# Kernel tuning notes

Measured on AMD Instinct MI355X. Metric: run time of the kernel, lower is better.

The kernel has to match this reference:

```python
import jax, jax.numpy as jnp
import numpy as np

B, S, D_MODEL, D_INNER = 64, 128, 1024, 1024


def setup_inputs() -> dict:
    key = jax.random.key(0)
    ks = jax.random.split(key, 10)
    sc = 0.02
    return {
        "embeddings": jax.random.normal(ks[0], (B, S, D_MODEL), dtype=jnp.float32),
        "Wq": jax.random.normal(ks[1], (D_MODEL, D_INNER), dtype=jnp.float32) * sc,
        "bq": jnp.zeros((D_INNER,), dtype=jnp.float32),
        "Wk": jax.random.normal(ks[2], (D_MODEL, D_INNER), dtype=jnp.float32) * sc,
        "bk": jnp.zeros((D_INNER,), dtype=jnp.float32),
        "Wv": jax.random.normal(ks[3], (D_MODEL, D_INNER), dtype=jnp.float32) * sc,
        "bv": jnp.zeros((D_INNER,), dtype=jnp.float32),
        "w": jax.random.normal(ks[4], (S, S), dtype=jnp.float32) * sc,
        "Wo": jax.random.normal(ks[5], (D_INNER, D_MODEL), dtype=jnp.float32) * sc,
        "bo": jnp.zeros((D_MODEL,), dtype=jnp.float32),
    }


def reference(embeddings, Wq, bq, Wk, bk, Wv, bv, w, Wo, bo):
    # embeddings: [B, S, Dm]
    seq_len = embeddings.shape[1]
    q = embeddings @ Wq + bq          # [B, S, Di]
    k = embeddings @ Wk + bk
    v = embeddings @ Wv + bv

    max_k = jnp.max(k, axis=1, keepdims=True)   # [B, 1, Di]
    exp_k = jnp.exp(k - max_k)                  # [B, S, Di]

    max_w = jnp.max(w, axis=1, keepdims=True)   # [S, 1]
    wn = w - max_w                              # [S, S]
    tril = jnp.tril(jnp.ones((seq_len, seq_len), dtype=bool))
    wn = jnp.where(tril, wn[:seq_len, :seq_len], -jnp.inf)
    # torch.einsum('bjj,bjd->bjd', exp_w, x) picks the DIAGONAL of exp_w
    # (repeated subscript j) and multiplies elementwise along the seq dim.
    diag_w = jnp.exp(jnp.diagonal(wn))          # [S]; tril diagonal is True so finite
    dw = diag_w[None, :, None]                  # [1, S, 1]

    numerator = dw * (exp_k * v)                # [B, S, Di]
    denominator = dw * exp_k                    # [B, S, Di]
    out = jax.nn.sigmoid(q) * (numerator / denominator)
    return out @ Wo + bo                        # [B, S, Dm]
```

## Files before the change

### kernel.cpp

```cpp
#include <hip/hip_runtime.h>


typedef short bf16x8 __attribute__((ext_vector_type(8)));
typedef float f32x4  __attribute__((ext_vector_type(4)));

__device__ __forceinline__ short f2bf(float f) {
  union { float f; unsigned u; } x; x.f = f;
  unsigned r = x.u + 0x7fffu + ((x.u >> 16) & 1u);
  return (short)(r >> 16);
}

struct alignas(16) S8 { short v[8]; };

#define GLDS(g, l) \
  __builtin_amdgcn_global_load_lds((const __attribute__((address_space(1))) void*)(g), \
                                   (__attribute__((address_space(3))) void*)(l), 16, 0, 0)

__global__ __launch_bounds__(256) void prep_kernel(
    const float* __restrict__ emb, const float* __restrict__ Wq, const float* __restrict__ Wv,
    const float* __restrict__ Wo, short* __restrict__ embB, short* __restrict__ WqvT,
    short* __restrict__ WoT) {
  __shared__ float tr[32 * 33];
  const int t = threadIdx.x;
  const int bid = blockIdx.x;
  const int gdim = gridDim.x;

  for (size_t i = (size_t)bid * 256 + t; i < 1048576; i += (size_t)gdim * 256) {
    const float4* p = (const float4*)emb + i * 2;
    float4 a = p[0], b = p[1];
    S8 s;
    s.v[0] = f2bf(a.x); s.v[1] = f2bf(a.y); s.v[2] = f2bf(a.z); s.v[3] = f2bf(a.w);
    s.v[4] = f2bf(b.x); s.v[5] = f2bf(b.y); s.v[6] = f2bf(b.z); s.v[7] = f2bf(b.w);
    ((S8*)embB)[i] = s;
  }

  int tx = t & 31, ty = t >> 5;
  for (int z = bid; z < 3072; z += gdim) {
    const float* in = (z < 1024) ? Wq : (z < 2048) ? Wv : Wo;
    short* op = (z < 1024) ? WqvT : (z < 2048) ? (WqvT + 1048576) : WoT;
    int ti = z & 1023;
    int bx = (ti & 31) * 32, by = (ti >> 5) * 32;
    __syncthreads();
#pragma unroll
    for (int i = 0; i < 32; i += 8)
      tr[(ty + i) * 33 + tx] = in[(size_t)(by + ty + i) * 1024 + bx + tx];
    __syncthreads();
#pragma unroll
    for (int i = 0; i < 32; i += 8)
      op[(size_t)(bx + ty + i) * 1024 + by + tx] = f2bf(tr[tx * 33 + ty + i]);
  }
}

__global__ __launch_bounds__(256) void gemm_qv_kernel(
    const short* __restrict__ A, const short* __restrict__ BT,
    const float* __restrict__ bq, const float* __restrict__ bv, short* __restrict__ X) {
  __shared__ short As[128 * 64];
  __shared__ short Bqs[64 * 64];
  __shared__ short Bvs[64 * 64];
  const int t = threadIdx.x;
  const int lane = t & 63;
  const int w = t >> 6;
  const int l16 = lane & 15;
  const int quad = lane >> 4;
  const int bm = blockIdx.x * 128;
  const int bn = blockIdx.y * 64;
  const int wm = (w & 1) * 64;
  const int wn = (w >> 1) * 32;

  const int r8 = t >> 3;
  const int swe = ((t & 7) ^ (r8 & 7)) * 8;
  const short* pA0 = A + (size_t)(bm + r8) * 1024 + swe;
  const short* pA1 = pA0 + 32 * 1024;
  const short* pA2 = pA0 + 64 * 1024;
  const short* pA3 = pA0 + 96 * 1024;
  const short* pBq0 = BT + (size_t)(bn + r8) * 1024 + swe;
  const short* pBq1 = pBq0 + 32 * 1024;
  const short* pBv0 = BT + (size_t)(1024 + bn + r8) * 1024 + swe;
  const short* pBv1 = pBv0 + 32 * 1024;
  short* lA = As + w * 512;
  short* lBq = Bqs + w * 512;
  short* lBv = Bvs + w * 512;

  const int qsw0 = (quad ^ (l16 & 7)) * 8;
  const int qsw1 = ((quad + 4) ^ (l16 & 7)) * 8;
  const short* fA0 = As + (wm + l16) * 64 + qsw0;
  const short* fA1 = As + (wm + l16) * 64 + qsw1;
  const short* fq0 = Bqs + (wn + l16) * 64 + qsw0;
  const short* fq1 = Bqs + (wn + l16) * 64 + qsw1;
  const short* fv0 = Bvs + (wn + l16) * 64 + qsw0;
  const short* fv1 = Bvs + (wn + l16) * 64 + qsw1;

  f32x4 accq[4][2] = {};
  f32x4 accv[4][2] = {};

  for (int it = 0; it < 16; ++it) {
    GLDS(pA0, lA); GLDS(pA1, lA + 2048); GLDS(pA2, lA + 4096); GLDS(pA3, lA + 6144);
    GLDS(pBq0, lBq); GLDS(pBq1, lBq + 2048);
    GLDS(pBv0, lBv); GLDS(pBv1, lBv + 2048);
    pA0 += 64; pA1 += 64; pA2 += 64; pA3 += 64;
    pBq0 += 64; pBq1 += 64; pBv0 += 64; pBv1 += 64;
    __syncthreads();

#pragma unroll
    for (int h = 0; h < 2; h++) {
      const short* fA = h ? fA1 : fA0;
      const short* fq = h ? fq1 : fq0;
      const short* fv = h ? fv1 : fv0;
      bf16x8 av[4], bqf[2], bvf[2];
#pragma unroll
      for (int i = 0; i < 4; i++) av[i] = *(const bf16x8*)(fA + i * 1024);
#pragma unroll
      for (int j = 0; j < 2; j++) {
        bqf[j] = *(const bf16x8*)(fq + j * 1024);
        bvf[j] = *(const bf16x8*)(fv + j * 1024);
      }
#pragma unroll
      for (int i = 0; i < 4; i++)
#pragma unroll
        for (int j = 0; j < 2; j++) {
          accq[i][j] = __builtin_amdgcn_mfma_f32_16x16x32_bf16(av[i], bqf[j], accq[i][j], 0, 0, 0);
          accv[i][j] = __builtin_amdgcn_mfma_f32_16x16x32_bf16(av[i], bvf[j], accv[i][j], 0, 0, 0);
        }
    }
    __syncthreads();
  }

#pragma unroll
  for (int j = 0; j < 2; j++) {
    int col = bn + wn + j * 16 + l16;
    float bql = bq[col], bvl = bv[col];
#pragma unroll
    for (int i = 0; i < 4; i++)
#pragma unroll
      for (int r = 0; r < 4; r++) {
        int row = bm + wm + i * 16 + quad * 4 + r;
        float q = accq[i][j][r] + bql;
        float v = accv[i][j][r] + bvl;
        float s = 1.0f / (1.0f + __expf(-q));
        X[(size_t)row * 1024 + col] = f2bf(s * v);
      }
  }
}

__global__ __launch_bounds__(256) void gemm_bt_kernel(
    const short* __restrict__ A, const short* __restrict__ BT, float* __restrict__ C,
    const float* __restrict__ bias) {
  __shared__ short As[128 * 64];
  __shared__ short Bs[128 * 64];
  const int t = threadIdx.x;
  const int lane = t & 63;
  const int w = t >> 6;
  const int l16 = lane & 15;
  const int quad = lane >> 4;
  const int bm = blockIdx.x * 128;
  const int bn = blockIdx.y * 128;
  const int wm = (w & 1) * 64;
  const int wn = (w >> 1) * 64;

  const int r8 = t >> 3;
  const int swe = ((t & 7) ^ (r8 & 7)) * 8;
  const short* pA0 = A + (size_t)(bm + r8) * 1024 + swe;
  const short* pA1 = pA0 + 32 * 1024;
  const short* pA2 = pA0 + 64 * 1024;
  const short* pA3 = pA0 + 96 * 1024;
  const short* pB0 = BT + (size_t)(bn + r8) * 1024 + swe;
  const short* pB1 = pB0 + 32 * 1024;
  const short* pB2 = pB0 + 64 * 1024;
  const short* pB3 = pB0 + 96 * 1024;
  short* lA = As + w * 512;
  short* lB = Bs + w * 512;

  const int qsw0 = (quad ^ (l16 & 7)) * 8;
  const int qsw1 = ((quad + 4) ^ (l16 & 7)) * 8;
  const short* fA0 = As + (wm + l16) * 64 + qsw0;
  const short* fA1 = As + (wm + l16) * 64 + qsw1;
  const short* fB0 = Bs + (wn + l16) * 64 + qsw0;
  const short* fB1 = Bs + (wn + l16) * 64 + qsw1;

  f32x4 acc[4][4] = {};

  for (int it = 0; it < 16; ++it) {
    GLDS(pA0, lA); GLDS(pA1, lA + 2048); GLDS(pA2, lA + 4096); GLDS(pA3, lA + 6144);
    GLDS(pB0, lB); GLDS(pB1, lB + 2048); GLDS(pB2, lB + 4096); GLDS(pB3, lB + 6144);
    pA0 += 64; pA1 += 64; pA2 += 64; pA3 += 64;
    pB0 += 64; pB1 += 64; pB2 += 64; pB3 += 64;
    __syncthreads();

#pragma unroll
    for (int h = 0; h < 2; h++) {
      const short* fA = h ? fA1 : fA0;
      const short* fB = h ? fB1 : fB0;
      bf16x8 av[4], bw[4];
#pragma unroll
      for (int i = 0; i < 4; i++) av[i] = *(const bf16x8*)(fA + i * 1024);
#pragma unroll
      for (int j = 0; j < 4; j++) bw[j] = *(const bf16x8*)(fB + j * 1024);
#pragma unroll
      for (int i = 0; i < 4; i++)
#pragma unroll
        for (int j = 0; j < 4; j++)
          acc[i][j] = __builtin_amdgcn_mfma_f32_16x16x32_bf16(av[i], bw[j], acc[i][j], 0, 0, 0);
    }
    __syncthreads();
  }

#pragma unroll
  for (int j = 0; j < 4; j++) {
    int col = bn + wn + j * 16 + l16;
    float bl = bias[col];
#pragma unroll
    for (int i = 0; i < 4; i++)
#pragma unroll
      for (int r = 0; r < 4; r++) {
        int row = bm + wm + i * 16 + quad * 4 + r;
        C[(size_t)row * 1024 + col] = acc[i][j][r] + bl;
      }
  }
}

extern "C" void kernel_launch(void* const* d_in, const int* in_sizes, int n_in,
                              void* d_out, int out_size, void* d_ws, size_t ws_size,
                              hipStream_t stream) {
  const float* emb = (const float*)d_in[0];
  const float* Wq  = (const float*)d_in[1];
  const float* bq  = (const float*)d_in[2];
  const float* Wv  = (const float*)d_in[5];
  const float* bv  = (const float*)d_in[6];
  const float* Wo  = (const float*)d_in[8];
  const float* bo  = (const float*)d_in[9];
  float* out = (float*)d_out;

  char* ws = (char*)d_ws;
  short* embB = (short*)(ws);
  short* X    = (short*)(ws + 16777216);
  short* WqvT = (short*)(ws + 33554432);
  short* WoT  = (short*)(ws + 37748736);

  prep_kernel<<<1024, 256, 0, stream>>>(emb, Wq, Wv, Wo, embB, WqvT, WoT);
  gemm_qv_kernel<<<dim3(64, 16), 256, 0, stream>>>(embB, WqvT, bq, bv, X);
  gemm_bt_kernel<<<dim3(64, 8), 256, 0, stream>>>(X, WoT, out, bo);
}
```

Before: 168.2 us.

## Double-buffer GEMM loads with larger 256x128 tiles, 8 waves and ping-pong scheduling

Both GEMM kernels now use 256x128 output tiles with 512 threads, a two-stage LDS double buffer fed by async global-to-LDS loads, and explicit vmcnt waits. The inner loop is split into barrier-separated MFMA phases that raise wave priority, and a swizzled block index groups tiles for L2 reuse. The aim is to hide global load latency behind MFMA work and cut per-tile load traffic. In exchange, LDS use rises to 128KB per block in the QV kernel and register pressure goes up, which can limit occupancy. The grid shrinks to 256 blocks, which may underfill the CUs.

```diff
diff --git a/kernel.cpp b/kernel.cpp
--- a/kernel.cpp
+++ b/kernel.cpp
@@ -15,6 +15,12 @@
 #define GLDS(g, l) \
   __builtin_amdgcn_global_load_lds((const __attribute__((address_space(1))) void*)(g), \
                                    (__attribute__((address_space(3))) void*)(l), 16, 0, 0)
+#define BAR()    __builtin_amdgcn_s_barrier()
+#define PRIO(x)  __builtin_amdgcn_s_setprio(x)
+#define SCHED0() __builtin_amdgcn_sched_barrier(0)
+#define VMCNT(N) asm volatile("s_waitcnt vmcnt(" #N ")" ::: "memory")
+#define LGKM0()  asm volatile("s_waitcnt lgkmcnt(0)" ::: "memory")
+#define MFMA(a, b, c) __builtin_amdgcn_mfma_f32_16x16x32_bf16((a), (b), (c), 0, 0, 0)
 
 __global__ __launch_bounds__(256) void prep_kernel(
     const float* __restrict__ emb, const float* __restrict__ Wq, const float* __restrict__ Wv,
@@ -51,169 +57,237 @@
   }
 }
 
-__global__ __launch_bounds__(256) void gemm_qv_kernel(
+__global__ __launch_bounds__(512, 2) void gemm_qv_kernel(
     const short* __restrict__ A, const short* __restrict__ BT,
     const float* __restrict__ bq, const float* __restrict__ bv, short* __restrict__ X) {
-  __shared__ short As[128 * 64];
-  __shared__ short Bqs[64 * 64];
-  __shared__ short Bvs[64 * 64];
+  __shared__ short As[2][256 * 64];
+  __shared__ short Bqs[2][128 * 64];
+  __shared__ short Bvs[2][128 * 64];
   const int t = threadIdx.x;
   const int lane = t & 63;
   const int w = t >> 6;
   const int l16 = lane & 15;
   const int quad = lane >> 4;
-  const int bm = blockIdx.x * 128;
-  const int bn = blockIdx.y * 64;
-  const int wm = (w & 1) * 64;
-  const int wn = (w >> 1) * 32;
+  const int b = blockIdx.x;
+  const int wg = (b & 7) * 32 + (b >> 3);
+  const int bm = (wg >> 3) * 256;
+  const int bn = (wg & 7) * 128;
+  const int wm = (w & 3) * 64;
+  const int wn = (w >> 2) * 64;
 
   const int r8 = t >> 3;
   const int swe = ((t & 7) ^ (r8 & 7)) * 8;
-  const short* pA0 = A + (size_t)(bm + r8) * 1024 + swe;
-  const short* pA1 = pA0 + 32 * 1024;
-  const short* pA2 = pA0 + 64 * 1024;
-  const short* pA3 = pA0 + 96 * 1024;
-  const short* pBq0 = BT + (size_t)(bn + r8) * 1024 + swe;
-  const short* pBq1 = pBq0 + 32 * 1024;
-  const short* pBv0 = BT + (size_t)(1024 + bn + r8) * 1024 + swe;
-  const short* pBv1 = pBv0 + 32 * 1024;
-  short* lA = As + w * 512;
-  short* lBq = Bqs + w * 512;
-  short* lBv = Bvs + w * 512;
-
-  const int qsw0 = (quad ^ (l16 & 7)) * 8;
-  const int qsw1 = ((quad + 4) ^ (l16 & 7)) * 8;
-  const short* fA0 = As + (wm + l16) * 64 + qsw0;
-  const short* fA1 = As + (wm + l16) * 64 + qsw1;
-  const short* fq0 = Bqs + (wn + l16) * 64 + qsw0;
-  const short* fq1 = Bqs + (wn + l16) * 64 + qsw1;
-  const short* fv0 = Bvs + (wn + l16) * 64 + qsw0;
-  const short* fv1 = Bvs + (wn + l16) * 64 + qsw1;
-
-  f32x4 accq[4][2] = {};
-  f32x4 accv[4][2] = {};
-
-  for (int it = 0; it < 16; ++it) {
-    GLDS(pA0, lA); GLDS(pA1, lA + 2048); GLDS(pA2, lA + 4096); GLDS(pA3, lA + 6144);
-    GLDS(pBq0, lBq); GLDS(pBq1, lBq + 2048);
-    GLDS(pBv0, lBv); GLDS(pBv1, lBv + 2048);
-    pA0 += 64; pA1 += 64; pA2 += 64; pA3 += 64;
-    pBq0 += 64; pBq1 += 64; pBv0 += 64; pBv1 += 64;
-    __syncthreads();
-
-#pragma unroll
-    for (int h = 0; h < 2; h++) {
-      const short* fA = h ? fA1 : fA0;
-      const short* fq = h ? fq1 : fq0;
-      const short* fv = h ? fv1 : fv0;
-      bf16x8 av[4], bqf[2], bvf[2];
-#pragma unroll
-      for (int i = 0; i < 4; i++) av[i] = *(const bf16x8*)(fA + i * 1024);
-#pragma unroll
-      for (int j = 0; j < 2; j++) {
-        bqf[j] = *(const bf16x8*)(fq + j * 1024);
-        bvf[j] = *(const bf16x8*)(fv + j * 1024);
-      }
-#pragma unroll
-      for (int i = 0; i < 4; i++)
-#pragma unroll
-        for (int j = 0; j < 2; j++) {
-          accq[i][j] = __builtin_amdgcn_mfma_f32_16x16x32_bf16(av[i], bqf[j], accq[i][j], 0, 0, 0);
-          accv[i][j] = __builtin_amdgcn_mfma_f32_16x16x32_bf16(av[i], bvf[j], accv[i][j], 0, 0, 0);
-        }
+  const short* gA = A + (size_t)(bm + r8) * 1024 + swe;
+  const short* gq = BT + (size_t)(bn + r8) * 1024 + swe;
+  const short* gv = BT + (size_t)(1024 + bn + r8) * 1024 + swe;
+  short* lA = &As[0][0] + w * 512;
+  short* lq = &Bqs[0][0] + w * 512;
+  short* lv = &Bvs[0][0] + w * 512;
+
+#define QV_STAGE(k, s) do {                                             \
+    const short* a_ = gA + (k) * 64; short* la_ = lA + (s) * 16384;     \
+    GLDS(a_, la_);               GLDS(a_ + 64 * 1024, la_ + 4096);      \
+    GLDS(a_ + 128 * 1024, la_ + 8192); GLDS(a_ + 192 * 1024, la_ + 12288); \
+    const short* q_ = gq + (k) * 64; short* lq_ = lq + (s) * 8192;      \
+    GLDS(q_, lq_);               GLDS(q_ + 64 * 1024, lq_ + 4096);      \
+    const short* v_ = gv + (k) * 64; short* lv_ = lv + (s) * 8192;      \
+    GLDS(v_, lv_);               GLDS(v_ + 64 * 1024, lv_ + 4096);      \
+  } while (0)
+
+  const int csw0 = (quad ^ (l16 & 7)) * 8;
+  const int csw1 = ((quad + 4) ^ (l16 & 7)) * 8;
+  const short* fA0 = &As[0][0] + (wm + l16) * 64 + csw0;
+  const short* fA1 = &As[0][0] + (wm + l16) * 64 + csw1;
+  const short* fq0 = &Bqs[0][0] + (wn + l16) * 64 + csw0;
+  const short* fq1 = &Bqs[0][0] + (wn + l16) * 64 + csw1;
+  const short* fv0 = &Bvs[0][0] + (wn + l16) * 64 + csw0;
+  const short* fv1 = &Bvs[0][0] + (wn + l16) * 64 + csw1;
+
+  f32x4 aq[4][4] = {};
+  f32x4 av[4][4] = {};
+
+  QV_STAGE(0, 0);
+  QV_STAGE(1, 1);
+
+  for (int j = 0; j < 16; ++j) {
+    const int s = j & 1;
+    const short* sA0 = fA0 + s * 16384;
+    const short* sA1 = fA1 + s * 16384;
+    const short* sq0 = fq0 + s * 8192;
+    const short* sq1 = fq1 + s * 8192;
+    const short* sv0 = fv0 + s * 8192;
+    const short* sv1 = fv1 + s * 8192;
+
+    if (j < 15) { VMCNT(8); } else { VMCNT(0); }
+    BAR();
+
+    bf16x8 a0[4], a1[4], b0[2], b1[2];
+#pragma unroll
+    for (int i = 0; i < 4; ++i) {
+      a0[i] = *(const bf16x8*)(sA0 + i * 1024);
+      a1[i] = *(const bf16x8*)(sA1 + i * 1024);
     }
-    __syncthreads();
-  }
-
-#pragma unroll
-  for (int j = 0; j < 2; j++) {
-    int col = bn + wn + j * 16 + l16;
-    float bql = bq[col], bvl = bv[col];
-#pragma unroll
-    for (int i = 0; i < 4; i++)
-#pragma unroll
-      for (int r = 0; r < 4; r++) {
-        int row = bm + wm + i * 16 + quad * 4 + r;
-        float q = accq[i][j][r] + bql;
-        float v = accv[i][j][r] + bvl;
-        float s = 1.0f / (1.0f + __expf(-q));
-        X[(size_t)row * 1024 + col] = f2bf(s * v);
-      }
-  }
-}
-
-__global__ __launch_bounds__(256) void gemm_bt_kernel(
+    b0[0] = *(const bf16x8*)(sq0);        b0[1] = *(const bf16x8*)(sq0 + 1024);
+    b1[0] = *(const bf16x8*)(sq1);        b1[1] = *(const bf16x8*)(sq1 + 1024);
+    BAR(); LGKM0(); SCHED0(); PRIO(1);
+#pragma unroll
+    for (int i = 0; i < 4; ++i)
+#pragma unroll
+      for (int n = 0; n < 2; ++n) {
+        aq[i][n] = MFMA(a0[i], b0[n], aq[i][n]);
+        aq[i][n] = MFMA(a1[i], b1[n], aq[i][n]);
+      }
+    PRIO(0); BAR();
+    b0[0] = *(const bf16x8*)(sq0 + 2048);  b0[1] = *(const bf16x8*)(sq0 + 3072);
+    b1[0] = *(const bf16x8*)(sq1 + 2048);  b1[1] = *(const bf16x8*)(sq1 + 3072);
+    BAR(); LGKM0(); SCHED0(); PRIO(1);
+#pragma unroll
+    for (int i = 0; i < 4; ++i)
+#pragma unroll
+      for (int n = 0; n < 2; ++n) {
+        aq[i][2 + n] = MFMA(a0[i], b0[n], aq[i][2 + n]);
+        aq[i][2 + n] = MFMA(a1[i], b1[n], aq[i][2 + n]);
+      }
+    PRIO(0); BAR();
+    b0[0] = *(const bf16x8*)(sv0);         b0[1] = *(const bf16x8*)(sv0 + 1024);
+    b1[0] = *(const bf16x8*)(sv1);         b1[1] = *(const bf16x8*)(sv1 + 1024);
+    BAR(); LGKM0(); SCHED0(); PRIO(1);
+#pragma unroll
+    for (int i = 0; i < 4; ++i)
+#pragma unroll
+      for (int n = 0; n < 2; ++n) {
+        av[i][n] = MFMA(a0[i], b0[n], av[i][n]);
+        av[i][n] = MFMA(a1[i], b1[n], av[i][n]);
+      }
+    PRIO(0); BAR();
+    b0[0] = *(const bf16x8*)(sv0 + 2048);  b0[1] = *(const bf16x8*)(sv0 + 3072);
+    b1[0] = *(const bf16x8*)(sv1 + 2048);  b1[1] = *(const bf16x8*)(sv1 + 3072);
+    BAR(); LGKM0(); SCHED0(); PRIO(1);
+#pragma unroll
+    for (int i = 0; i < 4; ++i)
+#pragma unroll
+      for (int n = 0; n < 2; ++n) {
+        av[i][2 + n] = MFMA(a0[i], b0[n], av[i][2 + n]);
+        av[i][2 + n] = MFMA(a1[i], b1[n], av[i][2 + n]);
+      }
+    PRIO(0); BAR();
+    if (j < 14) QV_STAGE(j + 2, s);
+  }
+#undef QV_STAGE
+
+#pragma unroll
+  for (int n = 0; n < 4; ++n) {
+    const int col = bn + wn + n * 16 + l16;
+    const float bql = bq[col], bvl = bv[col];
+#pragma unroll
+    for (int i = 0; i < 4; ++i)
+#pragma unroll
+      for (int r = 0; r < 4; ++r) {
+        const int row = bm + wm + i * 16 + quad * 4 + r;
+        const float q = aq[i][n][r] + bql;
+        const float v = av[i][n][r] + bvl;
+        const float sg = 1.0f / (1.0f + __expf(-q));
+        X[(size_t)row * 1024 + col] = f2bf(sg * v);
+      }
+  }
+}
+
+__global__ __launch_bounds__(512, 2) void gemm_bt_kernel(
     const short* __restrict__ A, const short* __restrict__ BT, float* __restrict__ C,
     const float* __restrict__ bias) {
-  __shared__ short As[128 * 64];
-  __shared__ short Bs[128 * 64];
+  __shared__ short As[2][256 * 64];
+  __shared__ short Bs[2][128 * 64];
   const int t = threadIdx.x;
   const int lane = t & 63;
   const int w = t >> 6;
   const int l16 = lane & 15;
   const int quad = lane >> 4;
-  const int bm = blockIdx.x * 128;
-  const int bn = blockIdx.y * 128;
-  const int wm = (w & 1) * 64;
-  const int wn = (w >> 1) * 64;
+  const int b = blockIdx.x;
+  const int wg = (b & 7) * 32 + (b >> 3);
+  const int bm = (wg >> 3) * 256;
+  const int bn = (wg & 7) * 128;
+  const int wm = (w & 3) * 64;
+  const int wn = (w >> 2) * 64;
 
   const int r8 = t >> 3;
   const int swe = ((t & 7) ^ (r8 & 7)) * 8;
-  const short* pA0 = A + (size_t)(bm + r8) * 1024 + swe;
-  const short* pA1 = pA0 + 32 * 1024;
-  const short* pA2 = pA0 + 64 * 1024;
-  const short* pA3 = pA0 + 96 * 1024;
-  const short* pB0 = BT + (size_t)(bn + r8) * 1024 + swe;
-  const short* pB1 = pB0 + 32 * 1024;
-  const short* pB2 = pB0 + 64 * 1024;
-  const short* pB3 = pB0 + 96 * 1024;
-  short* lA = As + w * 512;
-  short* lB = Bs + w * 512;
-
-  const int qsw0 = (quad ^ (l16 & 7)) * 8;
-  const int qsw1 = ((quad + 4) ^ (l16 & 7)) * 8;
-  const short* fA0 = As + (wm + l16) * 64 + qsw0;
-  const short* fA1 = As + (wm + l16) * 64 + qsw1;
-  const short* fB0 = Bs + (wn + l16) * 64 + qsw0;
-  const short* fB1 = Bs + (wn + l16) * 64 + qsw1;
+  const short* gA = A + (size_t)(bm + r8) * 1024 + swe;
+  const short* gB = BT + (size_t)(bn + r8) * 1024 + swe;
+  short* lA = &As[0][0] + w * 512;
+  short* lB = &Bs[0][0] + w * 512;
+
+#define BT_STAGE(k, s) do {                                             \
+    const short* a_ = gA + (k) * 64; short* la_ = lA + (s) * 16384;     \
+    GLDS(a_, la_);               GLDS(a_ + 64 * 1024, la_ + 4096);      \
+    GLDS(a_ + 128 * 1024, la_ + 8192); GLDS(a_ + 192 * 1024, la_ + 12288); \
+    const short* b_ = gB + (k) * 64; short* lb_ = lB + (s) * 8192;      \
+    GLDS(b_, lb_);               GLDS(b_ + 64 * 1024, lb_ + 4096);      \
+  } while (0)
+
+  const int csw0 = (quad ^ (l16 & 7)) * 8;
+  const int csw1 = ((quad + 4) ^ (l16 & 7)) * 8;
+  const short* fA0 = &As[0][0] + (wm + l16) * 64 + csw0;
+  const short* fA1 = &As[0][0] + (wm + l16) * 64 + csw1;
+  const short* fB0 = &Bs[0][0] + (wn + l16) * 64 + csw0;
+  const short* fB1 = &Bs[0][0] + (wn + l16) * 64 + csw1;
 
   f32x4 acc[4][4] = {};
 
-  for (int it = 0; it < 16; ++it) {
-    GLDS(pA0, lA); GLDS(pA1, lA + 2048); GLDS(pA2, lA + 4096); GLDS(pA3, lA + 6144);
-    GLDS(pB0, lB); GLDS(pB1, lB + 2048); GLDS(pB2, lB + 4096); GLDS(pB3, lB + 6144);
-    pA0 += 64; pA1 += 64; pA2 += 64; pA3 += 64;
-    pB0 += 64; pB1 += 64; pB2 += 64; pB3 += 64;
-    __syncthreads();
-
-#pragma unroll
-    for (int h = 0; h < 2; h++) {
-      const short* fA = h ? fA1 : fA0;
-      const short* fB = h ? fB1 : fB0;
-      bf16x8 av[4], bw[4];
-#pragma unroll
-      for (int i = 0; i < 4; i++) av[i] = *(const bf16x8*)(fA + i * 1024);
-#pragma unroll
-      for (int j = 0; j < 4; j++) bw[j] = *(const bf16x8*)(fB + j * 1024);
-#pragma unroll
-      for (int i = 0; i < 4; i++)
-#pragma unroll
-        for (int j = 0; j < 4; j++)
-          acc[i][j] = __builtin_amdgcn_mfma_f32_16x16x32_bf16(av[i], bw[j], acc[i][j], 0, 0, 0);
+  BT_STAGE(0, 0);
+  BT_STAGE(1, 1);
+
+  for (int j = 0; j < 16; ++j) {
+    const int s = j & 1;
+    const short* sA0 = fA0 + s * 16384;
+    const short* sA1 = fA1 + s * 16384;
+    const short* sB0 = fB0 + s * 8192;
+    const short* sB1 = fB1 + s * 8192;
+
+    if (j < 15) { VMCNT(6); } else { VMCNT(0); }
+    BAR();
+
+    bf16x8 a0[4], a1[4], b0[2], b1[2];
+#pragma unroll
+    for (int i = 0; i < 4; ++i) {
+      a0[i] = *(const bf16x8*)(sA0 + i * 1024);
+      a1[i] = *(const bf16x8*)(sA1 + i * 1024);
     }
-    __syncthreads();
-  }
-
-#pragma unroll
-  for (int j = 0; j < 4; j++) {
-    int col = bn + wn + j * 16 + l16;
-    float bl = bias[col];
-#pragma unroll
-    for (int i = 0; i < 4; i++)
-#pragma unroll
-      for (int r = 0; r < 4; r++) {
-        int row = bm + wm + i * 16 + quad * 4 + r;
-        C[(size_t)row * 1024 + col] = acc[i][j][r] + bl;
+    b0[0] = *(const bf16x8*)(sB0);        b0[1] = *(const bf16x8*)(sB0 + 1024);
+    b1[0] = *(const bf16x8*)(sB1);        b1[1] = *(const bf16x8*)(sB1 + 1024);
+    BAR(); LGKM0(); SCHED0(); PRIO(1);
+#pragma unroll
+    for (int i = 0; i < 4; ++i)
+#pragma unroll
+      for (int n = 0; n < 2; ++n) {
+        acc[i][n] = MFMA(a0[i], b0[n], acc[i][n]);
+        acc[i][n] = MFMA(a1[i], b1[n], acc[i][n]);
+      }
+    PRIO(0); BAR();
+    b0[0] = *(const bf16x8*)(sB0 + 2048);  b0[1] = *(const bf16x8*)(sB0 + 3072);
+    b1[0] = *(const bf16x8*)(sB1 + 2048);  b1[1] = *(const bf16x8*)(sB1 + 3072);
+    BAR(); LGKM0(); SCHED0(); PRIO(1);
+#pragma unroll
+    for (int i = 0; i < 4; ++i)
+#pragma unroll
+      for (int n = 0; n < 2; ++n) {
+        acc[i][2 + n] = MFMA(a0[i], b0[n], acc[i][2 + n]);
+        acc[i][2 + n] = MFMA(a1[i], b1[n], acc[i][2 + n]);
+      }
+    PRIO(0); BAR();
+    if (j < 14) BT_STAGE(j + 2, s);
+  }
+#undef BT_STAGE
+
+#pragma unroll
+  for (int n = 0; n < 4; ++n) {
+    const int col = bn + wn + n * 16 + l16;
+    const float bl = bias[col];
+#pragma unroll
+    for (int i = 0; i < 4; ++i)
+#pragma unroll
+      for (int r = 0; r < 4; ++r) {
+        const int row = bm + wm + i * 16 + quad * 4 + r;
+        C[(size_t)row * 1024 + col] = acc[i][n][r] + bl;
       }
   }
 }
@@ -237,6 +311,6 @@
   short* WoT  = (short*)(ws + 37748736);
 
   prep_kernel<<<1024, 256, 0, stream>>>(emb, Wq, Wv, Wo, embB, WqvT, WoT);
-  gemm_qv_kernel<<<dim3(64, 16), 256, 0, stream>>>(embB, WqvT, bq, bv, X);
-  gemm_bt_kernel<<<dim3(64, 8), 256, 0, stream>>>(X, WoT, out, bo);
-}
+  gemm_qv_kernel<<<256, 512, 0, stream>>>(embB, WqvT, bq, bv, X);
+  gemm_bt_kernel<<<256, 512, 0, stream>>>(X, WoT, out, bo);
+}
```

After: 173.9 us. 3.4% more time.
